# Optimization experiments

Measured on AMD Instinct MI355X. Metric: run time of the kernel, lower is better.

## Reference

```python
import jax, jax.numpy as jnp
import numpy as np

N_IN, N_OUT, RANK, RES_RANK, BATCH = 4096, 4096, 64, 4, 8192


def setup_inputs() -> dict:
    key = jax.random.key(0)
    kx, ku, kv, kur, kvr = jax.random.split(key, 5)
    return {
        "x": jax.random.normal(kx, (N_IN, BATCH), dtype=jnp.float32),
        "U": 0.02 * jax.random.normal(ku, (N_OUT, RANK), dtype=jnp.float32),
        "V": 0.02 * jax.random.normal(kv, (N_IN, RANK), dtype=jnp.float32),
        "U_res": 0.02 * jax.random.normal(kur, (N_OUT, RES_RANK), dtype=jnp.float32),
        "V_res": 0.02 * jax.random.normal(kvr, (N_IN, RES_RANK), dtype=jnp.float32),
        "active_cluster": 0,
    }


def reference(x, U, V, U_res, V_res, active_cluster):
    # W_core = U @ V.T  ->  (n_out, n_in); residual of the active cluster added in.
    # (active_cluster selects which residual factors are used; here the single
    #  provided U_res/V_res pair plays that role.)
    W = U @ V.T + U_res @ V_res.T          # (n_out, n_in)
    return jax.nn.relu(W @ x)              # (n_out, batch)
```

## Files before the change

### kernel.cpp

```cpp
#include <hip/hip_runtime.h>
#include <hip/hip_bf16.h>

#define N_IN    4096
#define N_OUT   4096
#define RANK    64
#define RES_RANK 4
#define RTOT    68
#define KPAD    96
#define BATCH   8192

typedef short bf16x8 __attribute__((ext_vector_type(8)));
typedef float f32x4  __attribute__((ext_vector_type(4)));
typedef float f32x2  __attribute__((ext_vector_type(2)));

__device__ inline short f2bf(float f) {
    __hip_bfloat16 h = __float2bfloat16(f);
    return *reinterpret_cast<short*>(&h);
}

__global__ __launch_bounds__(256) void phaseA_kernel(
    const float* __restrict__ x,
    const float* __restrict__ V,
    const float* __restrict__ Vr,
    float* __restrict__ t_part,
    int kchunk)
{
    __shared__ __align__(16) float sA[32][82];
    __shared__ __align__(16) float sB[32][130];
    const int tid  = threadIdx.x;
    const int lane = tid & 63;
    const int wv   = tid >> 6;
    const int ln15 = lane & 15;
    const int g    = lane >> 4;
    const int b0   = blockIdx.x * 128;
    const int ks   = blockIdx.y;
    const int k0   = ks * kchunk;

    f32x4 acc[5][2];
#pragma unroll
    for (int mt = 0; mt < 5; ++mt)
#pragma unroll
        for (int u = 0; u < 2; ++u)
            acc[mt][u] = (f32x4)0.0f;

    for (int i = tid; i < 32 * 14; i += 256) {
        int k = i / 14, c = i % 14;
        sA[k][68 + c] = 0.0f;
    }

    for (int kk = 0; kk < kchunk; kk += 32) {
        __syncthreads();

        {
            int k = tid >> 3, i0 = (tid & 7) * 8;
            const float* src = V + (size_t)(k0 + kk + k) * RANK + i0;
            float4 v0 = *(const float4*)(src);
            float4 v1 = *(const float4*)(src + 4);
            *(f32x2*)&sA[k][i0 + 0] = f32x2{v0.x, v0.y};
            *(f32x2*)&sA[k][i0 + 2] = f32x2{v0.z, v0.w};
            *(f32x2*)&sA[k][i0 + 4] = f32x2{v1.x, v1.y};
            *(f32x2*)&sA[k][i0 + 6] = f32x2{v1.z, v1.w};
        }
        if (tid < 32) {
            float4 vr = *(const float4*)(Vr + (size_t)(k0 + kk + tid) * RES_RANK);
            *(f32x2*)&sA[tid][64] = f32x2{vr.x, vr.y};
            *(f32x2*)&sA[tid][66] = f32x2{vr.z, vr.w};
        }
        {
            int kb  = lane >> 5;
            int col = (lane & 31) * 4;
#pragma unroll
            for (int c = 0; c < 4; ++c) {
                int k = wv * 8 + c * 2 + kb;
                float4 v = *(const float4*)(x + (size_t)(k0 + kk + k) * BATCH + b0 + col);
                *(f32x2*)&sB[k][col + 0] = f32x2{v.x, v.y};
                *(f32x2*)&sB[k][col + 2] = f32x2{v.z, v.w};
            }
        }
        __syncthreads();

        bf16x8 af[5], bfr[2];
#pragma unroll
        for (int mt = 0; mt < 5; ++mt) {
            int m = mt * 16 + ln15;
#pragma unroll
            for (int j = 0; j < 8; ++j)
                af[mt][j] = f2bf(sA[g * 8 + j][m]);
        }
#pragma unroll
        for (int u = 0; u < 2; ++u) {
            int n = (wv * 2 + u) * 16 + ln15;
#pragma unroll
            for (int j = 0; j < 8; ++j)
                bfr[u][j] = f2bf(sB[g * 8 + j][n]);
        }
#pragma unroll
        for (int mt = 0; mt < 5; ++mt)
#pragma unroll
            for (int u = 0; u < 2; ++u)
                acc[mt][u] = __builtin_amdgcn_mfma_f32_16x16x32_bf16(
                    af[mt], bfr[u], acc[mt][u], 0, 0, 0);
    }

#pragma unroll
    for (int mt = 0; mt < 5; ++mt)
#pragma unroll
        for (int u = 0; u < 2; ++u)
#pragma unroll
            for (int r = 0; r < 4; ++r) {
                int m = mt * 16 + g * 4 + r;
                if (m < RTOT) {
                    size_t off = ((size_t)ks * RTOT + m) * BATCH
                               + b0 + (wv * 2 + u) * 16 + ln15;
                    t_part[off] = acc[mt][u][r];
                }
            }
}

__global__ __launch_bounds__(256) void reduce_kernel(
    const float* __restrict__ t_part,
    unsigned short* __restrict__ t_bf16,
    int ksplit)
{
    __shared__ __align__(16) unsigned short sT[32][104];
    const int tid = threadIdx.x;
    const int b0  = blockIdx.x * 32;

    for (int i = tid; i < (32 * 104 * 2) / 16; i += 256)
        ((uint4*)sT)[i] = uint4{0, 0, 0, 0};
    __syncthreads();

    {
        int b  = tid & 31;
        int rq = tid >> 5;
        if (ksplit == 8) {
#pragma unroll 1
            for (int i = 0; i < 9; ++i) {
                int r = rq * 9 + i;
                if (r < RTOT) {
                    float s = 0.f;
#pragma unroll
                    for (int k = 0; k < 8; ++k)
                        s += t_part[((size_t)k * RTOT + r) * BATCH + b0 + b];
                    sT[b][r] = (unsigned short)f2bf(s);
                }
            }
        } else {
#pragma unroll 1
            for (int i = 0; i < 9; ++i) {
                int r = rq * 9 + i;
                if (r < RTOT) {
                    float s = 0.f;
                    for (int k = 0; k < ksplit; ++k)
                        s += t_part[((size_t)k * RTOT + r) * BATCH + b0 + b];
                    sT[b][r] = (unsigned short)f2bf(s);
                }
            }
        }
    }
    __syncthreads();

    {
        int b = tid >> 3, c = tid & 7;
        uint4 v = *(const uint4*)&sT[b][c * 8];
        *(uint4*)(t_bf16 + (size_t)(b0 + b) * KPAD + c * 8) = v;
        if (c < 4) {
            uint4 v2 = *(const uint4*)&sT[b][(c + 8) * 8];
            *(uint4*)(t_bf16 + (size_t)(b0 + b) * KPAD + (c + 8) * 8) = v2;
        }
    }
}

__global__ __launch_bounds__(256) void phaseB_kernel(
    const unsigned short* __restrict__ t_bf16,
    const float* __restrict__ U,
    const float* __restrict__ Ur,
    float* __restrict__ out)
{
    __shared__ __align__(16) unsigned short sU[128][104];
    __shared__ __align__(16) unsigned short sT[128][104];
    const int tid  = threadIdx.x;
    const int lane = tid & 63;
    const int wv   = tid >> 6;
    const int ln15 = lane & 15;
    const int g    = lane >> 4;
    const int b0   = blockIdx.x * 128;
    const int m0   = blockIdx.y * 128;

    {
        int m = tid >> 1, h = tid & 1;
        const float* src = U + (size_t)(m0 + m) * RANK + h * 32;
#pragma unroll
        for (int c = 0; c < 8; ++c) {
            float4 v = *(const float4*)(src + c * 4);
            union { unsigned short us[4]; uint2 u2; } p;
            p.us[0] = (unsigned short)f2bf(v.x);
            p.us[1] = (unsigned short)f2bf(v.y);
            p.us[2] = (unsigned short)f2bf(v.z);
            p.us[3] = (unsigned short)f2bf(v.w);
            *(uint2*)&sU[m][h * 32 + c * 4] = p.u2;
        }
    }
    if (tid < 128) {
        int m = tid;
        float4 v = *(const float4*)(Ur + (size_t)(m0 + m) * RES_RANK);
        union { unsigned short us[4]; uint2 u2; } p;
        p.us[0] = (unsigned short)f2bf(v.x);
        p.us[1] = (unsigned short)f2bf(v.y);
        p.us[2] = (unsigned short)f2bf(v.z);
        p.us[3] = (unsigned short)f2bf(v.w);
        *(uint2*)&sU[m][64] = p.u2;
        uint2 z{0, 0};
#pragma unroll
        for (int c = 0; c < 7; ++c)
            *(uint2*)&sU[m][68 + c * 4] = z;
    }
    {
        int n = tid >> 1, c6 = (tid & 1) * 6;
        const unsigned short* src = t_bf16 + (size_t)(b0 + n) * KPAD + c6 * 8;
#pragma unroll
        for (int i = 0; i < 6; ++i) {
            uint4 v = *(const uint4*)(src + i * 8);
            *(uint4*)&sT[n][(c6 + i) * 8] = v;
        }
    }
    __syncthreads();

    f32x4 acc[2][8];
#pragma unroll
    for (int q = 0; q < 2; ++q)
#pragma unroll
        for (int nt = 0; nt < 8; ++nt)
            acc[q][nt] = (f32x4)0.0f;

#pragma unroll
    for (int ks = 0; ks < 3; ++ks) {
        bf16x8 a[2], b[8];
#pragma unroll
        for (int q = 0; q < 2; ++q) {
            int m = (wv * 2 + q) * 16 + ln15;
            a[q] = *(const bf16x8*)&sU[m][ks * 32 + g * 8];
        }
#pragma unroll
        for (int nt = 0; nt < 8; ++nt) {
            int n = nt * 16 + ln15;
            b[nt] = *(const bf16x8*)&sT[n][ks * 32 + g * 8];
        }
#pragma unroll
        for (int q = 0; q < 2; ++q)
#pragma unroll
            for (int nt = 0; nt < 8; ++nt)
                acc[q][nt] = __builtin_amdgcn_mfma_f32_16x16x32_bf16(
                    a[q], b[nt], acc[q][nt], 0, 0, 0);
    }

#pragma unroll
    for (int q = 0; q < 2; ++q)
#pragma unroll
        for (int nt = 0; nt < 8; ++nt)
#pragma unroll
            for (int r = 0; r < 4; ++r) {
                int row = m0 + (wv * 2 + q) * 16 + g * 4 + r;
                int col = b0 + nt * 16 + ln15;
                out[(size_t)row * BATCH + col] = fmaxf(acc[q][nt][r], 0.0f);
            }
}

extern "C" void kernel_launch(void* const* d_in, const int* in_sizes, int n_in,
                              void* d_out, int out_size, void* d_ws, size_t ws_size,
                              hipStream_t stream)
{
    const float* x  = (const float*)d_in[0];
    const float* U  = (const float*)d_in[1];
    const float* V  = (const float*)d_in[2];
    const float* Ur = (const float*)d_in[3];
    const float* Vr = (const float*)d_in[4];
    float* out = (float*)d_out;

    int ksplit = 8;
    while (ksplit > 1 &&
           ws_size < (size_t)ksplit * RTOT * BATCH * 4 + (size_t)BATCH * KPAD * 2)
        ksplit >>= 1;
    const int kchunk = N_IN / ksplit;

    float* t_part = (float*)d_ws;
    unsigned short* t_bf16 =
        (unsigned short*)((char*)d_ws + (size_t)ksplit * RTOT * BATCH * 4);

    phaseA_kernel<<<dim3(BATCH / 128, ksplit), 256, 0, stream>>>(x, V, Vr, t_part, kchunk);
    reduce_kernel<<<dim3(BATCH / 32), 256, 0, stream>>>(t_part, t_bf16, ksplit);
    phaseB_kernel<<<dim3(BATCH / 128, N_OUT / 128), 256, 0, stream>>>(t_bf16, U, Ur, out);
}
```

Baseline: 262.0 us.

## Restructure phase A: stage V in LDS once, stream x into registers, KSPLIT 16

New measurement: 275.9 us. +5.3%, slower.

```diff
diff --git a/kernel.cpp b/kernel.cpp
--- a/kernel.cpp
+++ b/kernel.cpp
@@ -8,10 +8,12 @@
 #define RTOT    68
 #define KPAD    96
 #define BATCH   8192
+#define KSPLIT  16
+#define KCHUNK  256
+#define SVSTR   264
 
 typedef short bf16x8 __attribute__((ext_vector_type(8)));
 typedef float f32x4  __attribute__((ext_vector_type(4)));
-typedef float f32x2  __attribute__((ext_vector_type(2)));
 
 __device__ inline short f2bf(float f) {
     __hip_bfloat16 h = __float2bfloat16(f);
@@ -22,11 +24,9 @@
     const float* __restrict__ x,
     const float* __restrict__ V,
     const float* __restrict__ Vr,
-    float* __restrict__ t_part,
-    int kchunk)
-{
-    __shared__ __align__(16) float sA[32][82];
-    __shared__ __align__(16) float sB[32][130];
+    float* __restrict__ t_part)
+{
+    __shared__ __align__(16) unsigned short sV[80][SVSTR];
     const int tid  = threadIdx.x;
     const int lane = tid & 63;
     const int wv   = tid >> 6;
@@ -34,141 +34,93 @@
     const int g    = lane >> 4;
     const int b0   = blockIdx.x * 128;
     const int ks   = blockIdx.y;
-    const int k0   = ks * kchunk;
-
-    f32x4 acc[5][2];
-#pragma unroll
-    for (int mt = 0; mt < 5; ++mt)
-#pragma unroll
-        for (int u = 0; u < 2; ++u)
-            acc[mt][u] = (f32x4)0.0f;
-
-    for (int i = tid; i < 32 * 14; i += 256) {
-        int k = i / 14, c = i % 14;
-        sA[k][68 + c] = 0.0f;
-    }
-
-    for (int kk = 0; kk < kchunk; kk += 32) {
-        __syncthreads();
-
-        {
-            int k = tid >> 3, i0 = (tid & 7) * 8;
-            const float* src = V + (size_t)(k0 + kk + k) * RANK + i0;
-            float4 v0 = *(const float4*)(src);
-            float4 v1 = *(const float4*)(src + 4);
-            *(f32x2*)&sA[k][i0 + 0] = f32x2{v0.x, v0.y};
-            *(f32x2*)&sA[k][i0 + 2] = f32x2{v0.z, v0.w};
-            *(f32x2*)&sA[k][i0 + 4] = f32x2{v1.x, v1.y};
-            *(f32x2*)&sA[k][i0 + 6] = f32x2{v1.z, v1.w};
-        }
-        if (tid < 32) {
-            float4 vr = *(const float4*)(Vr + (size_t)(k0 + kk + tid) * RES_RANK);
-            *(f32x2*)&sA[tid][64] = f32x2{vr.x, vr.y};
-            *(f32x2*)&sA[tid][66] = f32x2{vr.z, vr.w};
-        }
-        {
-            int kb  = lane >> 5;
-            int col = (lane & 31) * 4;
-#pragma unroll
-            for (int c = 0; c < 4; ++c) {
-                int k = wv * 8 + c * 2 + kb;
-                float4 v = *(const float4*)(x + (size_t)(k0 + kk + k) * BATCH + b0 + col);
-                *(f32x2*)&sB[k][col + 0] = f32x2{v.x, v.y};
-                *(f32x2*)&sB[k][col + 2] = f32x2{v.z, v.w};
-            }
-        }
-        __syncthreads();
-
-        bf16x8 af[5], bfr[2];
-#pragma unroll
-        for (int mt = 0; mt < 5; ++mt) {
-            int m = mt * 16 + ln15;
-#pragma unroll
-            for (int j = 0; j < 8; ++j)
-                af[mt][j] = f2bf(sA[g * 8 + j][m]);
-        }
-#pragma unroll
-        for (int u = 0; u < 2; ++u) {
-            int n = (wv * 2 + u) * 16 + ln15;
-#pragma unroll
-            for (int j = 0; j < 8; ++j)
-                bfr[u][j] = f2bf(sB[g * 8 + j][n]);
-        }
-#pragma unroll
-        for (int mt = 0; mt < 5; ++mt)
-#pragma unroll
-            for (int u = 0; u < 2; ++u)
-                acc[mt][u] = __builtin_amdgcn_mfma_f32_16x16x32_bf16(
-                    af[mt], bfr[u], acc[mt][u], 0, 0, 0);
-    }
-
-#pragma unroll
-    for (int mt = 0; mt < 5; ++mt)
-#pragma unroll
-        for (int u = 0; u < 2; ++u)
+    const int k0   = ks * KCHUNK;
+
+    for (int i = tid; i < 12 * (SVSTR / 2); i += 256) {
+        int r = 68 + i / (SVSTR / 2), c = i % (SVSTR / 2);
+        *(unsigned int*)&sV[r][c * 2] = 0u;
+    }
+
+    {
+        const float* vrow = V + (size_t)(k0 + tid) * RANK;
+#pragma unroll
+        for (int c = 0; c < 16; ++c) {
+            float4 v = *(const float4*)(vrow + c * 4);
+            sV[c * 4 + 0][tid] = (unsigned short)f2bf(v.x);
+            sV[c * 4 + 1][tid] = (unsigned short)f2bf(v.y);
+            sV[c * 4 + 2][tid] = (unsigned short)f2bf(v.z);
+            sV[c * 4 + 3][tid] = (unsigned short)f2bf(v.w);
+        }
+        float4 vr4 = *(const float4*)(Vr + (size_t)(k0 + tid) * RES_RANK);
+        sV[64][tid] = (unsigned short)f2bf(vr4.x);
+        sV[65][tid] = (unsigned short)f2bf(vr4.y);
+        sV[66][tid] = (unsigned short)f2bf(vr4.z);
+        sV[67][tid] = (unsigned short)f2bf(vr4.w);
+    }
+    __syncthreads();
+
+    f32x4 acc[2][5];
+#pragma unroll
+    for (int q = 0; q < 2; ++q)
+#pragma unroll
+        for (int nt = 0; nt < 5; ++nt)
+            acc[q][nt] = (f32x4)0.0f;
+
+#pragma unroll 2
+    for (int kk = 0; kk < KCHUNK; kk += 32) {
+        bf16x8 a[2];
+#pragma unroll
+        for (int q = 0; q < 2; ++q) {
+            const float* xp = x + (size_t)(k0 + kk + g * 8) * BATCH
+                            + b0 + (wv * 2 + q) * 16 + ln15;
+            float f0 = xp[0 * BATCH], f1 = xp[1 * BATCH];
+            float f2 = xp[2 * BATCH], f3 = xp[3 * BATCH];
+            float f4 = xp[4 * BATCH], f5 = xp[5 * BATCH];
+            float f6 = xp[6 * BATCH], f7 = xp[7 * BATCH];
+            a[q][0] = f2bf(f0); a[q][1] = f2bf(f1);
+            a[q][2] = f2bf(f2); a[q][3] = f2bf(f3);
+            a[q][4] = f2bf(f4); a[q][5] = f2bf(f5);
+            a[q][6] = f2bf(f6); a[q][7] = f2bf(f7);
+        }
+        bf16x8 bfr[5];
+#pragma unroll
+        for (int nt = 0; nt < 5; ++nt)
+            bfr[nt] = *(const bf16x8*)&sV[nt * 16 + ln15][kk + g * 8];
+
+#pragma unroll
+        for (int q = 0; q < 2; ++q)
+#pragma unroll
+            for (int nt = 0; nt < 5; ++nt)
+                acc[q][nt] = __builtin_amdgcn_mfma_f32_16x16x32_bf16(
+                    a[q], bfr[nt], acc[q][nt], 0, 0, 0);
+    }
+
+#pragma unroll
+    for (int q = 0; q < 2; ++q)
+#pragma unroll
+        for (int nt = 0; nt < 5; ++nt)
 #pragma unroll
             for (int r = 0; r < 4; ++r) {
-                int m = mt * 16 + g * 4 + r;
-                if (m < RTOT) {
-                    size_t off = ((size_t)ks * RTOT + m) * BATCH
-                               + b0 + (wv * 2 + u) * 16 + ln15;
-                    t_part[off] = acc[mt][u][r];
-                }
+                int b  = b0 + (wv * 2 + q) * 16 + g * 4 + r;
+                int rr = nt * 16 + ln15;
+                if (rr < RTOT)
+                    t_part[((size_t)ks * BATCH + b) * RTOT + rr] = acc[q][nt][r];
             }
 }
 
 __global__ __launch_bounds__(256) void reduce_kernel(
     const float* __restrict__ t_part,
-    unsigned short* __restrict__ t_bf16,
-    int ksplit)
-{
-    __shared__ __align__(16) unsigned short sT[32][104];
-    const int tid = threadIdx.x;
-    const int b0  = blockIdx.x * 32;
-
-    for (int i = tid; i < (32 * 104 * 2) / 16; i += 256)
-        ((uint4*)sT)[i] = uint4{0, 0, 0, 0};
-    __syncthreads();
-
-    {
-        int b  = tid & 31;
-        int rq = tid >> 5;
-        if (ksplit == 8) {
-#pragma unroll 1
-            for (int i = 0; i < 9; ++i) {
-                int r = rq * 9 + i;
-                if (r < RTOT) {
-                    float s = 0.f;
-#pragma unroll
-                    for (int k = 0; k < 8; ++k)
-                        s += t_part[((size_t)k * RTOT + r) * BATCH + b0 + b];
-                    sT[b][r] = (unsigned short)f2bf(s);
-                }
-            }
-        } else {
-#pragma unroll 1
-            for (int i = 0; i < 9; ++i) {
-                int r = rq * 9 + i;
-                if (r < RTOT) {
-                    float s = 0.f;
-                    for (int k = 0; k < ksplit; ++k)
-                        s += t_part[((size_t)k * RTOT + r) * BATCH + b0 + b];
-                    sT[b][r] = (unsigned short)f2bf(s);
-                }
-            }
-        }
-    }
-    __syncthreads();
-
-    {
-        int b = tid >> 3, c = tid & 7;
-        uint4 v = *(const uint4*)&sT[b][c * 8];
-        *(uint4*)(t_bf16 + (size_t)(b0 + b) * KPAD + c * 8) = v;
-        if (c < 4) {
-            uint4 v2 = *(const uint4*)&sT[b][(c + 8) * 8];
-            *(uint4*)(t_bf16 + (size_t)(b0 + b) * KPAD + (c + 8) * 8) = v2;
-        }
-    }
+    unsigned short* __restrict__ t_bf16)
+{
+    const int i  = blockIdx.x * 256 + threadIdx.x;
+    const int b  = i / KPAD, rr = i % KPAD;
+    float s = 0.f;
+    if (rr < RTOT) {
+#pragma unroll
+        for (int k = 0; k < KSPLIT; ++k)
+            s += t_part[((size_t)k * BATCH + b) * RTOT + rr];
+    }
+    t_bf16[i] = (rr < RTOT) ? (unsigned short)f2bf(s) : (unsigned short)0;
 }
 
 __global__ __launch_bounds__(256) void phaseB_kernel(
@@ -277,17 +229,11 @@
     const float* Vr = (const float*)d_in[4];
     float* out = (float*)d_out;
 
-    int ksplit = 8;
-    while (ksplit > 1 &&
-           ws_size < (size_t)ksplit * RTOT * BATCH * 4 + (size_t)BATCH * KPAD * 2)
-        ksplit >>= 1;
-    const int kchunk = N_IN / ksplit;
-
     float* t_part = (float*)d_ws;
     unsigned short* t_bf16 =
-        (unsigned short*)((char*)d_ws + (size_t)ksplit * RTOT * BATCH * 4);
-
-    phaseA_kernel<<<dim3(BATCH / 128, ksplit), 256, 0, stream>>>(x, V, Vr, t_part, kchunk);
-    reduce_kernel<<<dim3(BATCH / 32), 256, 0, stream>>>(t_part, t_bf16, ksplit);
+        (unsigned short*)((char*)d_ws + (size_t)KSPLIT * BATCH * RTOT * 4);
+
+    phaseA_kernel<<<dim3(BATCH / 128, KSPLIT), 256, 0, stream>>>(x, V, Vr, t_part);
+    reduce_kernel<<<dim3((BATCH * KPAD) / 256), 256, 0, stream>>>(t_part, t_bf16);
     phaseB_kernel<<<dim3(BATCH / 128, N_OUT / 128), 256, 0, stream>>>(t_bf16, U, Ur, out);
 }
```
